# Kernel tuning notes

Hardware: AMD Instinct MI355X
Metric: run time of the kernel (lower is better)

## Reference

```python
import jax, jax.numpy as jnp
import numpy as np

HIDDEN = 896
NUM_Q_HEADS = 14
NUM_KV_HEADS = 2
HEAD_DIM = 64
ROPE_BASE = 10000.0
B, S = 4, 2048


def rotate_half(x):
    x1, x2 = jnp.split(x, 2, axis=-1)
    return jnp.concatenate((-x2, x1), axis=-1)


def rope_cos_sin(position_ids):
    # position_ids: [B, S] int -> cos/sin [B, 1, S, HEAD_DIM]
    inv_freq = 1.0 / (ROPE_BASE ** (jnp.arange(0, HEAD_DIM, 2, dtype=jnp.float32) / HEAD_DIM))
    freqs = position_ids.astype(jnp.float32)[..., None] * inv_freq  # [B,S,D/2]
    emb = jnp.concatenate((freqs, freqs), axis=-1)  # [B,S,D]
    return jnp.cos(emb)[:, None, :, :], jnp.sin(emb)[:, None, :, :]


def setup_inputs() -> dict:
    key = jax.random.key(0)
    k1, k2, k3, k4, k5 = jax.random.split(key, 5)
    s = 1.0 / np.sqrt(HIDDEN)
    return {
        "hidden_states": jax.random.normal(k1, (B, S, HIDDEN), dtype=jnp.float32),
        "position_ids": jnp.broadcast_to(jnp.arange(S, dtype=jnp.int64), (B, S)),
        "Wq": jax.random.normal(k2, (HIDDEN, NUM_Q_HEADS * HEAD_DIM), dtype=jnp.float32) * s,
        "Wk": jax.random.normal(k3, (HIDDEN, NUM_KV_HEADS * HEAD_DIM), dtype=jnp.float32) * s,
        "Wv": jax.random.normal(k4, (HIDDEN, NUM_KV_HEADS * HEAD_DIM), dtype=jnp.float32) * s,
        "Wo": jax.random.normal(k5, (NUM_Q_HEADS * HEAD_DIM, HIDDEN), dtype=jnp.float32) * s,
    }


def reference(hidden_states, position_ids, Wq, Wk, Wv, Wo):
    b, s, _ = hidden_states.shape
    n_rep = NUM_Q_HEADS // NUM_KV_HEADS

    q = (hidden_states @ Wq).reshape(b, s, NUM_Q_HEADS, HEAD_DIM).transpose(0, 2, 1, 3)   # [B,Hq,S,D]
    k = (hidden_states @ Wk).reshape(b, s, NUM_KV_HEADS, HEAD_DIM).transpose(0, 2, 1, 3)  # [B,Hkv,S,D]
    v = (hidden_states @ Wv).reshape(b, s, NUM_KV_HEADS, HEAD_DIM).transpose(0, 2, 1, 3)

    cos, sin = rope_cos_sin(position_ids)  # [B,1,S,D]
    q = q * cos + rotate_half(q) * sin
    k = k * cos + rotate_half(k) * sin

    # repeat_interleave KV heads to match query heads
    k = jnp.repeat(k, n_rep, axis=1)  # [B,Hq,S,D]
    v = jnp.repeat(v, n_rep, axis=1)

    scale = 1.0 / jnp.sqrt(jnp.float32(HEAD_DIM))
    attn = jnp.einsum('bhqd,bhkd->bhqk', q, k) * scale  # [B,Hq,S,S]
    attn = jax.nn.softmax(attn, axis=-1)
    out = jnp.einsum('bhqk,bhkd->bhqd', attn, v)  # [B,Hq,S,D]
    out = out.transpose(0, 2, 1, 3).reshape(b, s, NUM_Q_HEADS * HEAD_DIM)
    return out @ Wo
```

## Files before the change

kernel.cpp:

```cpp
#include <hip/hip_runtime.h>
#include <hip/hip_bf16.h>
#include <math.h>

typedef unsigned short ushort_t;
typedef __bf16 bf16x8 __attribute__((ext_vector_type(8)));
typedef float f32x4 __attribute__((ext_vector_type(4)));

#define HIDDEN 896
#define NQH 14
#define NKVH 2
#define HD 64
#define SEQ 2048
#define NBATCH 4

__device__ inline ushort_t f2bf(float x) {
  union { float f; unsigned u; } c; c.f = x;
  unsigned r = c.u + 0x7FFFu + ((c.u >> 16) & 1u);
  return (ushort_t)(r >> 16);
}

__device__ inline unsigned pack2bf(float a, float b) {
  union { float f; unsigned u; } ca, cb; ca.f = a; cb.f = b;
  unsigned ua = ca.u + 0x8000u, ub = cb.u + 0x8000u;
  return __builtin_amdgcn_perm(ub, ua, 0x07060302);
}

__device__ inline bf16x8 ldfrag(const ushort_t* p) {
  return *reinterpret_cast<const bf16x8*>(p);
}

__device__ inline void async16(const ushort_t* g, ushort_t* l) {
  __builtin_amdgcn_global_load_lds(
      (const __attribute__((address_space(1))) void*)g,
      (__attribute__((address_space(3))) void*)l, 16, 0, 0);
}


__global__ void k_convert(const float* __restrict__ in, ushort_t* __restrict__ out, int n4) {
  int i = blockIdx.x * blockDim.x + threadIdx.x;
  if (i >= n4) return;
  float4 v = reinterpret_cast<const float4*>(in)[i];
  ushort4 o;
  o.x = f2bf(v.x); o.y = f2bf(v.y); o.z = f2bf(v.z); o.w = f2bf(v.w);
  reinterpret_cast<ushort4*>(out)[i] = o;
}

__global__ void k_transpose(const float* __restrict__ in, ushort_t* __restrict__ out, int K, int N) {
  __shared__ float tile[32][33];
  int k0 = blockIdx.y * 32, n0 = blockIdx.x * 32;
  for (int r = threadIdx.y; r < 32; r += 8) {
    int k = k0 + r, n = n0 + threadIdx.x;
    tile[r][threadIdx.x] = (k < K && n < N) ? in[(size_t)k * N + n] : 0.f;
  }
  __syncthreads();
  for (int r = threadIdx.y; r < 32; r += 8) {
    int n = n0 + r, k = k0 + threadIdx.x;
    if (n < N && k < K) out[(size_t)n * K + k] = f2bf(tile[threadIdx.x][r]);
  }
}

__global__ __launch_bounds__(256) void k_qkv(
    const ushort_t* __restrict__ hb,
    const ushort_t* __restrict__ wqT,
    const ushort_t* __restrict__ wkT,
    const ushort_t* __restrict__ wvT,
    const int* __restrict__ pos_ids,
    ushort_t* __restrict__ Qg,
    ushort_t* __restrict__ Kg,
    ushort_t* __restrict__ Vtg) {
  __shared__ ushort_t sa[128 * 32];
  __shared__ ushort_t sb[64 * 32];
  __shared__ float cbuf[128 * 64];

  const int nt = blockIdx.x;
  const int m0 = blockIdx.y * 128;
  const int tid = threadIdx.x;
  const int wave = tid >> 6, lane = tid & 63;
  const int l15 = lane & 15, quad = lane >> 4;
  const int wm = wave >> 1, wn = wave & 1;

  const ushort_t* wsrc; int nsrc0;
  if (nt < 14)      { wsrc = wqT; nsrc0 = nt * 64; }
  else if (nt < 16) { wsrc = wkT; nsrc0 = (nt - 14) * 64; }
  else              { wsrc = wvT; nsrc0 = (nt - 16) * 64; }

  f32x4 acc[4][2];
  const f32x4 z4 = {0.f, 0.f, 0.f, 0.f};
#pragma unroll
  for (int a = 0; a < 4; ++a)
#pragma unroll
    for (int b = 0; b < 2; ++b) acc[a][b] = z4;

  for (int kt = 0; kt < 28; ++kt) {
    const int k0 = kt * 32;
    __syncthreads();
#pragma unroll
    for (int i = 0; i < 2; ++i) {
      int c = wave * 128 + i * 64 + lane;
      async16(hb + (size_t)(m0 + (c >> 2)) * HIDDEN + k0 + (c & 3) * 8,
              sa + (size_t)(wave * 128 + i * 64) * 8);
    }
    {
      int c = wave * 64 + lane;
      async16(wsrc + (size_t)(nsrc0 + (c >> 2)) * HIDDEN + k0 + (c & 3) * 8,
              sb + (size_t)(wave * 64) * 8);
    }
    __syncthreads();
    bf16x8 bf0 = ldfrag(sb + ((wn * 32 + l15) * 32 + quad * 8));
    bf16x8 bf1 = ldfrag(sb + ((wn * 32 + 16 + l15) * 32 + quad * 8));
#pragma unroll
    for (int mb = 0; mb < 4; ++mb) {
      bf16x8 af = ldfrag(sa + ((wm * 64 + mb * 16 + l15) * 32 + quad * 8));
      acc[mb][0] = __builtin_amdgcn_mfma_f32_16x16x32_bf16(af, bf0, acc[mb][0], 0, 0, 0);
      acc[mb][1] = __builtin_amdgcn_mfma_f32_16x16x32_bf16(af, bf1, acc[mb][1], 0, 0, 0);
    }
  }

  __syncthreads();
#pragma unroll
  for (int mb = 0; mb < 4; ++mb)
#pragma unroll
    for (int nb = 0; nb < 2; ++nb)
#pragma unroll
      for (int r = 0; r < 4; ++r)
        cbuf[(wm * 64 + mb * 16 + quad * 4 + r) * 64 + wn * 32 + nb * 16 + l15] = acc[mb][nb][r];
  __syncthreads();

  if (nt < 16) {
    const float cs = 0.125f * 1.44269504088896f;
    for (int p = tid; p < 128 * 32; p += 256) {
      int row = p >> 5, d = p & 31;
      int token = m0 + row;
      int b = token >> 11, s = token & 2047;
      int pos = pos_ids[token];
      float x0 = cbuf[row * 64 + d];
      float x1 = cbuf[row * 64 + d + 32];
      float inv = exp2f(-(float)d * 0.41524101186092596f);
      float ang = (float)pos * inv;
      float sn, cn;
      sincosf(ang, &sn, &cn);
      float y0 = x0 * cn - x1 * sn;
      float y1 = x1 * cn + x0 * sn;
      if (nt < 14) {
        size_t base = ((size_t)(b * NQH + nt) * SEQ + s) * HD;
        Qg[base + d]      = f2bf(y0 * cs);
        Qg[base + d + 32] = f2bf(y1 * cs);
      } else {
        size_t base = ((size_t)(b * NKVH + (nt - 14)) * SEQ + s) * HD;
        Kg[base + d]      = f2bf(y0);
        Kg[base + d + 32] = f2bf(y1);
      }
    }
  } else {
    int kvh = nt - 16;
    for (int p = tid; p < 128 * 64; p += 256) {
      int srow = p & 127, d = p >> 7;
      int token = m0 + srow;
      int b = token >> 11, s = token & 2047;
      Vtg[((size_t)(b * NKVH + kvh) * HD + d) * SEQ + s] = f2bf(cbuf[srow * 64 + d]);
    }
  }
}

__global__ __launch_bounds__(256) void k_attn(
    const ushort_t* __restrict__ Qg,
    const ushort_t* __restrict__ Kg,
    const ushort_t* __restrict__ Vtg,
    ushort_t* __restrict__ attn) {
  __shared__ ushort_t kbuf[64 * 64];
  __shared__ ushort_t vbuf[64 * 64];
  __shared__ ushort_t pbuf[4][32 * 72];

  const int qt = blockIdx.x;
  const int bh = blockIdx.y;
  const int b = bh / NQH, h = bh % NQH;
  const int kvh = h / (NQH / NKVH);
  const int tid = threadIdx.x;
  const int wave = tid >> 6, lane = tid & 63;
  const int l15 = lane & 15, quad = lane >> 4;
  const int q0 = qt * 128;

  bf16x8 qf[2][2];
#pragma unroll
  for (int qs = 0; qs < 2; ++qs) {
    const size_t qb = ((size_t)bh * SEQ + q0 + wave * 32 + qs * 16 + l15) * HD + quad * 8;
    qf[qs][0] = ldfrag(Qg + qb);
    qf[qs][1] = ldfrag(Qg + qb + 32);
  }

  const size_t kbase = (size_t)(b * NKVH + kvh) * SEQ * HD;
  const size_t vbase = (size_t)(b * NKVH + kvh) * HD * SEQ;

  float l_acc[2] = {0.f, 0.f};
  f32x4 o[2][4];
  const f32x4 z4 = {0.f, 0.f, 0.f, 0.f};
#pragma unroll
  for (int qs = 0; qs < 2; ++qs)
#pragma unroll
    for (int nb = 0; nb < 4; ++nb) o[qs][nb] = z4;

  ushort_t* pw = pbuf[wave];

  for (int jt = 0; jt < 32; ++jt) {
    const int s0 = jt * 64;
    __syncthreads();
#pragma unroll
    for (int i = 0; i < 2; ++i) {
      int s = i * 256 + tid;
      int row = s >> 3;
      int c = (s & 7) ^ (row & 7);
      int sbase = i * 256 + wave * 64;
      async16(Kg + kbase + (size_t)(s0 + row) * HD + c * 8, kbuf + sbase * 8);
      async16(Vtg + vbase + (size_t)row * SEQ + s0 + c * 8, vbuf + sbase * 8);
    }
    __syncthreads();

    float lsum[2] = {0.f, 0.f};
#pragma unroll
    for (int nb = 0; nb < 4; ++nb) {
      int row = nb * 16 + l15;
      int sw = row & 7;
      bf16x8 kf0 = ldfrag(kbuf + (row * 8 + (quad ^ sw)) * 8);
      bf16x8 kf1 = ldfrag(kbuf + (row * 8 + ((4 + quad) ^ sw)) * 8);
#pragma unroll
      for (int qs = 0; qs < 2; ++qs) {
        f32x4 t = z4;
        t = __builtin_amdgcn_mfma_f32_16x16x32_bf16(kf0, qf[qs][0], t, 0, 0, 0);
        t = __builtin_amdgcn_mfma_f32_16x16x32_bf16(kf1, qf[qs][1], t, 0, 0, 0);
        float p0 = __builtin_amdgcn_exp2f(t[0]);
        float p1 = __builtin_amdgcn_exp2f(t[1]);
        float p2 = __builtin_amdgcn_exp2f(t[2]);
        float p3 = __builtin_amdgcn_exp2f(t[3]);
        lsum[qs] += (p0 + p1) + (p2 + p3);
        uint2 d;
        d.x = pack2bf(p0, p1);
        d.y = pack2bf(p2, p3);
        *reinterpret_cast<uint2*>(pw + (qs * 16 + l15) * 72 + nb * 16 + quad * 4) = d;
      }
    }
#pragma unroll
    for (int qs = 0; qs < 2; ++qs) {
      float s = lsum[qs];
      s += __shfl_xor(s, 16);
      s += __shfl_xor(s, 32);
      l_acc[qs] += s;
    }

    bf16x8 pf[2][2];
#pragma unroll
    for (int qs = 0; qs < 2; ++qs) {
      pf[qs][0] = ldfrag(pw + (qs * 16 + l15) * 72 + quad * 8);
      pf[qs][1] = ldfrag(pw + (qs * 16 + l15) * 72 + 32 + quad * 8);
    }
#pragma unroll
    for (int nb = 0; nb < 4; ++nb) {
      int row = nb * 16 + l15;
      int sw = row & 7;
      bf16x8 vf0 = ldfrag(vbuf + (row * 8 + (quad ^ sw)) * 8);
      bf16x8 vf1 = ldfrag(vbuf + (row * 8 + ((4 + quad) ^ sw)) * 8);
#pragma unroll
      for (int qs = 0; qs < 2; ++qs) {
        o[qs][nb] = __builtin_amdgcn_mfma_f32_16x16x32_bf16(pf[qs][0], vf0, o[qs][nb], 0, 0, 0);
        o[qs][nb] = __builtin_amdgcn_mfma_f32_16x16x32_bf16(pf[qs][1], vf1, o[qs][nb], 0, 0, 0);
      }
    }
  }

#pragma unroll
  for (int qs = 0; qs < 2; ++qs) {
    float il = 1.0f / l_acc[qs];
#pragma unroll
    for (int r = 0; r < 4; ++r) {
      float inv = __shfl(il, quad * 4 + r);
      int qg = q0 + wave * 32 + qs * 16 + quad * 4 + r;
#pragma unroll
      for (int nb = 0; nb < 4; ++nb) {
        float val = o[qs][nb][r] * inv;
        attn[(size_t)(b * SEQ + qg) * (NQH * HD) + h * HD + nb * 16 + l15] = f2bf(val);
      }
    }
  }
}

__global__ __launch_bounds__(256) void k_oproj(
    const ushort_t* __restrict__ attn,
    const ushort_t* __restrict__ woT,
    float* __restrict__ out) {
  __shared__ ushort_t sa[128 * 32];
  __shared__ ushort_t sb[64 * 32];

  const int n0 = blockIdx.x * 64;
  const int m0 = blockIdx.y * 128;
  const int tid = threadIdx.x;
  const int wave = tid >> 6, lane = tid & 63;
  const int l15 = lane & 15, quad = lane >> 4;
  const int wm = wave >> 1, wn = wave & 1;

  f32x4 acc[4][2];
  const f32x4 z4 = {0.f, 0.f, 0.f, 0.f};
#pragma unroll
  for (int a = 0; a < 4; ++a)
#pragma unroll
    for (int b = 0; b < 2; ++b) acc[a][b] = z4;

  for (int kt = 0; kt < 28; ++kt) {
    const int k0 = kt * 32;
    __syncthreads();
#pragma unroll
    for (int i = 0; i < 2; ++i) {
      int c = wave * 128 + i * 64 + lane;
      async16(attn + (size_t)(m0 + (c >> 2)) * HIDDEN + k0 + (c & 3) * 8,
              sa + (size_t)(wave * 128 + i * 64) * 8);
    }
    {
      int c = wave * 64 + lane;
      async16(woT + (size_t)(n0 + (c >> 2)) * HIDDEN + k0 + (c & 3) * 8,
              sb + (size_t)(wave * 64) * 8);
    }
    __syncthreads();
    bf16x8 bf0 = ldfrag(sb + ((wn * 32 + l15) * 32 + quad * 8));
    bf16x8 bf1 = ldfrag(sb + ((wn * 32 + 16 + l15) * 32 + quad * 8));
#pragma unroll
    for (int mb = 0; mb < 4; ++mb) {
      bf16x8 af = ldfrag(sa + ((wm * 64 + mb * 16 + l15) * 32 + quad * 8));
      acc[mb][0] = __builtin_amdgcn_mfma_f32_16x16x32_bf16(af, bf0, acc[mb][0], 0, 0, 0);
      acc[mb][1] = __builtin_amdgcn_mfma_f32_16x16x32_bf16(af, bf1, acc[mb][1], 0, 0, 0);
    }
  }

#pragma unroll
  for (int mb = 0; mb < 4; ++mb)
#pragma unroll
    for (int nb = 0; nb < 2; ++nb)
#pragma unroll
      for (int r = 0; r < 4; ++r)
        out[(size_t)(m0 + wm * 64 + mb * 16 + quad * 4 + r) * HIDDEN +
            n0 + wn * 32 + nb * 16 + l15] = acc[mb][nb][r];
}


extern "C" void kernel_launch(void* const* d_in, const int* in_sizes, int n_in,
                              void* d_out, int out_size, void* d_ws, size_t ws_size,
                              hipStream_t stream) {
  (void)in_sizes; (void)n_in; (void)out_size; (void)ws_size;
  const float* hidden = (const float*)d_in[0];
  const int* pos      = (const int*)d_in[1];
  const float* Wq     = (const float*)d_in[2];
  const float* Wk     = (const float*)d_in[3];
  const float* Wv     = (const float*)d_in[4];
  const float* Wo     = (const float*)d_in[5];
  float* out = (float*)d_out;

  char* ws = (char*)d_ws;
  ushort_t* hb   = (ushort_t*)(ws);
  ushort_t* wqT  = (ushort_t*)(ws + 14680064);
  ushort_t* wkT  = (ushort_t*)(ws + 16285696);
  ushort_t* wvT  = (ushort_t*)(ws + 16515072);
  ushort_t* woT  = (ushort_t*)(ws + 16744448);
  ushort_t* Qg   = (ushort_t*)(ws + 18350080);
  ushort_t* Kg   = (ushort_t*)(ws + 33030144);
  ushort_t* Vtg  = (ushort_t*)(ws + 35127296);
  ushort_t* attn = (ushort_t*)(ws + 37224448);

  k_convert<<<7168, 256, 0, stream>>>(hidden, hb, 1835008);
  dim3 tb(32, 8);
  k_transpose<<<dim3(28, 28), tb, 0, stream>>>(Wq, wqT, 896, 896);
  k_transpose<<<dim3(4, 28), tb, 0, stream>>>(Wk, wkT, 896, 128);
  k_transpose<<<dim3(4, 28), tb, 0, stream>>>(Wv, wvT, 896, 128);
  k_transpose<<<dim3(28, 28), tb, 0, stream>>>(Wo, woT, 896, 896);

  k_qkv<<<dim3(18, 64), 256, 0, stream>>>(hb, wqT, wkT, wvT, pos, Qg, Kg, Vtg);
  k_attn<<<dim3(16, 56), 256, 0, stream>>>(Qg, Kg, Vtg, attn);
  k_oproj<<<dim3(14, 64), 256, 0, stream>>>(attn, woT, out);
}
```

Baseline: 269.8 us.

## Merge prep kernels, widen GEMM tiles, use RoPE table, double-buffer attention KV

Folds the conversion and all weight transposes into one launch that also precomputes a cos/sin table. The QKV and output-projection GEMMs move to 128x128 tiles, and the QKV epilogue applies RoPE straight from registers, dropping the LDS staging buffer and the per-element sincos. Attention now double-buffers its K/V tiles so the next tile loads while the current one is computed, and defers the row-sum reduction to the end. The aim is fewer launches, more reuse per tile and less load latency, in exchange for higher register and LDS pressure that could lower occupancy. The cos/sin table is indexed by the pos value and holds only 2048 entries, so position ids outside that range would read past it.

```diff
diff --git a/kernel.cpp b/kernel.cpp
--- a/kernel.cpp
+++ b/kernel.cpp
@@ -36,18 +36,10 @@
 }
 
 
-__global__ void k_convert(const float* __restrict__ in, ushort_t* __restrict__ out, int n4) {
-  int i = blockIdx.x * blockDim.x + threadIdx.x;
-  if (i >= n4) return;
-  float4 v = reinterpret_cast<const float4*>(in)[i];
-  ushort4 o;
-  o.x = f2bf(v.x); o.y = f2bf(v.y); o.z = f2bf(v.z); o.w = f2bf(v.w);
-  reinterpret_cast<ushort4*>(out)[i] = o;
-}
-
-__global__ void k_transpose(const float* __restrict__ in, ushort_t* __restrict__ out, int K, int N) {
+__device__ inline void transpose_sec(const float* __restrict__ in, ushort_t* __restrict__ out,
+                                     int K, int N, int bx, int by) {
   __shared__ float tile[32][33];
-  int k0 = blockIdx.y * 32, n0 = blockIdx.x * 32;
+  int k0 = by * 32, n0 = bx * 32;
   for (int r = threadIdx.y; r < 32; r += 8) {
     int k = k0 + r, n = n0 + threadIdx.x;
     tile[r][threadIdx.x] = (k < K && n < N) ? in[(size_t)k * N + n] : 0.f;
@@ -59,37 +51,67 @@
   }
 }
 
+__global__ void k_prep(const float* __restrict__ hidden, ushort_t* __restrict__ hb,
+                       const float* __restrict__ Wq, const float* __restrict__ Wk,
+                       const float* __restrict__ Wv, const float* __restrict__ Wo,
+                       ushort_t* __restrict__ wT, ushort_t* __restrict__ woT,
+                       float2* __restrict__ ctab) {
+  const int blk = blockIdx.x;
+  const int tid = threadIdx.y * 32 + threadIdx.x;
+  if (blk < 7168) {
+    int i = blk * 256 + tid;
+    float4 v = reinterpret_cast<const float4*>(hidden)[i];
+    ushort4 o;
+    o.x = f2bf(v.x); o.y = f2bf(v.y); o.z = f2bf(v.z); o.w = f2bf(v.w);
+    reinterpret_cast<ushort4*>(hb)[i] = o;
+  } else if (blk < 7424) {
+    int idx = (blk - 7168) * 256 + tid;
+    int s = idx >> 5, dp = idx & 31;
+    float inv = exp2f(-(float)dp * 0.41524101186092596f);
+    float ang = (float)s * inv;
+    float sn, cn;
+    sincosf(ang, &sn, &cn);
+    ctab[idx] = make_float2(cn, sn);
+  } else if (blk < 8208) {
+    int t = blk - 7424;
+    transpose_sec(Wq, wT, 896, 896, t % 28, t / 28);
+  } else if (blk < 8320) {
+    int t = blk - 8208;
+    transpose_sec(Wk, wT + (size_t)896 * 896, 896, 128, t % 4, t / 4);
+  } else if (blk < 8432) {
+    int t = blk - 8320;
+    transpose_sec(Wv, wT + (size_t)1024 * 896, 896, 128, t % 4, t / 4);
+  } else {
+    int t = blk - 8432;
+    transpose_sec(Wo, woT, 896, 896, t % 28, t / 28);
+  }
+}
+
 __global__ __launch_bounds__(256) void k_qkv(
     const ushort_t* __restrict__ hb,
-    const ushort_t* __restrict__ wqT,
-    const ushort_t* __restrict__ wkT,
-    const ushort_t* __restrict__ wvT,
+    const ushort_t* __restrict__ wT,
     const int* __restrict__ pos_ids,
+    const float2* __restrict__ ctab,
     ushort_t* __restrict__ Qg,
     ushort_t* __restrict__ Kg,
     ushort_t* __restrict__ Vtg) {
   __shared__ ushort_t sa[128 * 32];
-  __shared__ ushort_t sb[64 * 32];
-  __shared__ float cbuf[128 * 64];
-
-  const int nt = blockIdx.x;
+  __shared__ ushort_t sbb[128 * 32];
+
+  const int sect = blockIdx.x;
+  const int nt0 = sect * 128;
   const int m0 = blockIdx.y * 128;
   const int tid = threadIdx.x;
   const int wave = tid >> 6, lane = tid & 63;
   const int l15 = lane & 15, quad = lane >> 4;
   const int wm = wave >> 1, wn = wave & 1;
 
-  const ushort_t* wsrc; int nsrc0;
-  if (nt < 14)      { wsrc = wqT; nsrc0 = nt * 64; }
-  else if (nt < 16) { wsrc = wkT; nsrc0 = (nt - 14) * 64; }
-  else              { wsrc = wvT; nsrc0 = (nt - 16) * 64; }
-
-  f32x4 acc[4][2];
+  f32x4 acc[4][4];
   const f32x4 z4 = {0.f, 0.f, 0.f, 0.f};
 #pragma unroll
   for (int a = 0; a < 4; ++a)
 #pragma unroll
-    for (int b = 0; b < 2; ++b) acc[a][b] = z4;
+    for (int b = 0; b < 4; ++b) acc[a][b] = z4;
 
   for (int kt = 0; kt < 28; ++kt) {
     const int k0 = kt * 32;
@@ -99,65 +121,62 @@
       int c = wave * 128 + i * 64 + lane;
       async16(hb + (size_t)(m0 + (c >> 2)) * HIDDEN + k0 + (c & 3) * 8,
               sa + (size_t)(wave * 128 + i * 64) * 8);
-    }
-    {
-      int c = wave * 64 + lane;
-      async16(wsrc + (size_t)(nsrc0 + (c >> 2)) * HIDDEN + k0 + (c & 3) * 8,
-              sb + (size_t)(wave * 64) * 8);
+      async16(wT + (size_t)(nt0 + (c >> 2)) * HIDDEN + k0 + (c & 3) * 8,
+              sbb + (size_t)(wave * 128 + i * 64) * 8);
     }
     __syncthreads();
-    bf16x8 bf0 = ldfrag(sb + ((wn * 32 + l15) * 32 + quad * 8));
-    bf16x8 bf1 = ldfrag(sb + ((wn * 32 + 16 + l15) * 32 + quad * 8));
+    bf16x8 bf[4], af[4];
+#pragma unroll
+    for (int nb = 0; nb < 4; ++nb)
+      bf[nb] = ldfrag(sbb + ((wn * 64 + nb * 16 + l15) * 32 + quad * 8));
+#pragma unroll
+    for (int mb = 0; mb < 4; ++mb)
+      af[mb] = ldfrag(sa + ((wm * 64 + mb * 16 + l15) * 32 + quad * 8));
+#pragma unroll
+    for (int mb = 0; mb < 4; ++mb)
+#pragma unroll
+      for (int nb = 0; nb < 4; ++nb)
+        acc[mb][nb] = __builtin_amdgcn_mfma_f32_16x16x32_bf16(af[mb], bf[nb], acc[mb][nb], 0, 0, 0);
+  }
+
+  if (sect < 8) {
+    const bool isQ = sect < 7;
+    const float csc = isQ ? 0.125f * 1.4426950408889634f : 1.0f;
+    ushort_t* dst = isQ ? Qg : Kg;
+    const int nheads = isQ ? NQH : NKVH;
+    const int hh = isQ ? sect * 2 + wn : wn;
+#pragma unroll
+    for (int mb = 0; mb < 4; ++mb)
+#pragma unroll
+      for (int r = 0; r < 4; ++r) {
+        int token = m0 + wm * 64 + mb * 16 + quad * 4 + r;
+        int b = token >> 11, s = token & 2047;
+        int pos = pos_ids[token];
+        size_t base = ((size_t)(b * nheads + hh) * SEQ + s) * HD;
+#pragma unroll
+        for (int nb = 0; nb < 2; ++nb) {
+          float2 cs = ctab[pos * 32 + nb * 16 + l15];
+          float x0 = acc[mb][nb][r];
+          float x1 = acc[mb][nb + 2][r];
+          float y0 = (x0 * cs.x - x1 * cs.y) * csc;
+          float y1 = (x1 * cs.x + x0 * cs.y) * csc;
+          dst[base + nb * 16 + l15]      = f2bf(y0);
+          dst[base + nb * 16 + l15 + 32] = f2bf(y1);
+        }
+      }
+  } else {
 #pragma unroll
     for (int mb = 0; mb < 4; ++mb) {
-      bf16x8 af = ldfrag(sa + ((wm * 64 + mb * 16 + l15) * 32 + quad * 8));
-      acc[mb][0] = __builtin_amdgcn_mfma_f32_16x16x32_bf16(af, bf0, acc[mb][0], 0, 0, 0);
-      acc[mb][1] = __builtin_amdgcn_mfma_f32_16x16x32_bf16(af, bf1, acc[mb][1], 0, 0, 0);
-    }
-  }
-
-  __syncthreads();
-#pragma unroll
-  for (int mb = 0; mb < 4; ++mb)
-#pragma unroll
-    for (int nb = 0; nb < 2; ++nb)
-#pragma unroll
-      for (int r = 0; r < 4; ++r)
-        cbuf[(wm * 64 + mb * 16 + quad * 4 + r) * 64 + wn * 32 + nb * 16 + l15] = acc[mb][nb][r];
-  __syncthreads();
-
-  if (nt < 16) {
-    const float cs = 0.125f * 1.44269504088896f;
-    for (int p = tid; p < 128 * 32; p += 256) {
-      int row = p >> 5, d = p & 31;
-      int token = m0 + row;
-      int b = token >> 11, s = token & 2047;
-      int pos = pos_ids[token];
-      float x0 = cbuf[row * 64 + d];
-      float x1 = cbuf[row * 64 + d + 32];
-      float inv = exp2f(-(float)d * 0.41524101186092596f);
-      float ang = (float)pos * inv;
-      float sn, cn;
-      sincosf(ang, &sn, &cn);
-      float y0 = x0 * cn - x1 * sn;
-      float y1 = x1 * cn + x0 * sn;
-      if (nt < 14) {
-        size_t base = ((size_t)(b * NQH + nt) * SEQ + s) * HD;
-        Qg[base + d]      = f2bf(y0 * cs);
-        Qg[base + d + 32] = f2bf(y1 * cs);
-      } else {
-        size_t base = ((size_t)(b * NKVH + (nt - 14)) * SEQ + s) * HD;
-        Kg[base + d]      = f2bf(y0);
-        Kg[base + d + 32] = f2bf(y1);
+      int token0 = m0 + wm * 64 + mb * 16 + quad * 4;
+      int b = token0 >> 11, s = token0 & 2047;
+#pragma unroll
+      for (int nb = 0; nb < 4; ++nb) {
+        int d = nb * 16 + l15;
+        uint2 pk;
+        pk.x = pack2bf(acc[mb][nb][0], acc[mb][nb][1]);
+        pk.y = pack2bf(acc[mb][nb][2], acc[mb][nb][3]);
+        *reinterpret_cast<uint2*>(Vtg + ((size_t)(b * NKVH + wn) * HD + d) * SEQ + s) = pk;
       }
-    }
-  } else {
-    int kvh = nt - 16;
-    for (int p = tid; p < 128 * 64; p += 256) {
-      int srow = p & 127, d = p >> 7;
-      int token = m0 + srow;
-      int b = token >> 11, s = token & 2047;
-      Vtg[((size_t)(b * NKVH + kvh) * HD + d) * SEQ + s] = f2bf(cbuf[srow * 64 + d]);
     }
   }
 }
@@ -167,8 +186,8 @@
     const ushort_t* __restrict__ Kg,
     const ushort_t* __restrict__ Vtg,
     ushort_t* __restrict__ attn) {
-  __shared__ ushort_t kbuf[64 * 64];
-  __shared__ ushort_t vbuf[64 * 64];
+  __shared__ ushort_t kbuf[2][64 * 64];
+  __shared__ ushort_t vbuf[2][64 * 64];
   __shared__ ushort_t pbuf[4][32 * 72];
 
   const int qt = blockIdx.x;
@@ -191,7 +210,14 @@
   const size_t kbase = (size_t)(b * NKVH + kvh) * SEQ * HD;
   const size_t vbase = (size_t)(b * NKVH + kvh) * HD * SEQ;
 
-  float l_acc[2] = {0.f, 0.f};
+  const int srow = tid >> 3;
+  const int sc0 = (tid & 7) ^ (srow & 7);
+  const int srow2 = (256 + tid) >> 3;
+  const int sc2 = (tid & 7) ^ (srow2 & 7);
+  const int sbase1 = wave * 64 * 8;
+  const int sbase2 = (256 + wave * 64) * 8;
+
+  float l_part[2] = {0.f, 0.f};
   f32x4 o[2][4];
   const f32x4 z4 = {0.f, 0.f, 0.f, 0.f};
 #pragma unroll
@@ -201,27 +227,32 @@
 
   ushort_t* pw = pbuf[wave];
 
+  async16(Kg + kbase + (size_t)srow * HD + sc0 * 8, kbuf[0] + sbase1);
+  async16(Vtg + vbase + (size_t)srow * SEQ + sc0 * 8, vbuf[0] + sbase1);
+  async16(Kg + kbase + (size_t)srow2 * HD + sc2 * 8, kbuf[0] + sbase2);
+  async16(Vtg + vbase + (size_t)srow2 * SEQ + sc2 * 8, vbuf[0] + sbase2);
+
   for (int jt = 0; jt < 32; ++jt) {
-    const int s0 = jt * 64;
+    const int cur = jt & 1;
     __syncthreads();
-#pragma unroll
-    for (int i = 0; i < 2; ++i) {
-      int s = i * 256 + tid;
-      int row = s >> 3;
-      int c = (s & 7) ^ (row & 7);
-      int sbase = i * 256 + wave * 64;
-      async16(Kg + kbase + (size_t)(s0 + row) * HD + c * 8, kbuf + sbase * 8);
-      async16(Vtg + vbase + (size_t)row * SEQ + s0 + c * 8, vbuf + sbase * 8);
-    }
-    __syncthreads();
-
-    float lsum[2] = {0.f, 0.f};
+    if (jt + 1 < 32) {
+      const int nxt = cur ^ 1;
+      const int s1 = (jt + 1) * 64;
+      async16(Kg + kbase + (size_t)(s1 + srow) * HD + sc0 * 8, kbuf[nxt] + sbase1);
+      async16(Vtg + vbase + (size_t)srow * SEQ + s1 + sc0 * 8, vbuf[nxt] + sbase1);
+      async16(Kg + kbase + (size_t)(s1 + srow2) * HD + sc2 * 8, kbuf[nxt] + sbase2);
+      async16(Vtg + vbase + (size_t)srow2 * SEQ + s1 + sc2 * 8, vbuf[nxt] + sbase2);
+    }
+
+    const ushort_t* kb = kbuf[cur];
+    const ushort_t* vb = vbuf[cur];
+
 #pragma unroll
     for (int nb = 0; nb < 4; ++nb) {
       int row = nb * 16 + l15;
       int sw = row & 7;
-      bf16x8 kf0 = ldfrag(kbuf + (row * 8 + (quad ^ sw)) * 8);
-      bf16x8 kf1 = ldfrag(kbuf + (row * 8 + ((4 + quad) ^ sw)) * 8);
+      bf16x8 kf0 = ldfrag(kb + (row * 8 + (quad ^ sw)) * 8);
+      bf16x8 kf1 = ldfrag(kb + (row * 8 + ((4 + quad) ^ sw)) * 8);
 #pragma unroll
       for (int qs = 0; qs < 2; ++qs) {
         f32x4 t = z4;
@@ -231,20 +262,13 @@
         float p1 = __builtin_amdgcn_exp2f(t[1]);
         float p2 = __builtin_amdgcn_exp2f(t[2]);
         float p3 = __builtin_amdgcn_exp2f(t[3]);
-        lsum[qs] += (p0 + p1) + (p2 + p3);
+        l_part[qs] += (p0 + p1) + (p2 + p3);
         uint2 d;
         d.x = pack2bf(p0, p1);
         d.y = pack2bf(p2, p3);
         *reinterpret_cast<uint2*>(pw + (qs * 16 + l15) * 72 + nb * 16 + quad * 4) = d;
       }
     }
-#pragma unroll
-    for (int qs = 0; qs < 2; ++qs) {
-      float s = lsum[qs];
-      s += __shfl_xor(s, 16);
-      s += __shfl_xor(s, 32);
-      l_acc[qs] += s;
-    }
 
     bf16x8 pf[2][2];
 #pragma unroll
@@ -256,8 +280,8 @@
     for (int nb = 0; nb < 4; ++nb) {
       int row = nb * 16 + l15;
       int sw = row & 7;
-      bf16x8 vf0 = ldfrag(vbuf + (row * 8 + (quad ^ sw)) * 8);
-      bf16x8 vf1 = ldfrag(vbuf + (row * 8 + ((4 + quad) ^ sw)) * 8);
+      bf16x8 vf0 = ldfrag(vb + (row * 8 + (quad ^ sw)) * 8);
+      bf16x8 vf1 = ldfrag(vb + (row * 8 + ((4 + quad) ^ sw)) * 8);
 #pragma unroll
       for (int qs = 0; qs < 2; ++qs) {
         o[qs][nb] = __builtin_amdgcn_mfma_f32_16x16x32_bf16(pf[qs][0], vf0, o[qs][nb], 0, 0, 0);
@@ -268,7 +292,15 @@
 
 #pragma unroll
   for (int qs = 0; qs < 2; ++qs) {
-    float il = 1.0f / l_acc[qs];
+    float s = l_part[qs];
+    s += __shfl_xor(s, 16);
+    s += __shfl_xor(s, 32);
+    l_part[qs] = s;
+  }
+
+#pragma unroll
+  for (int qs = 0; qs < 2; ++qs) {
+    float il = 1.0f / l_part[qs];
 #pragma unroll
     for (int r = 0; r < 4; ++r) {
       float inv = __shfl(il, quad * 4 + r);
@@ -287,21 +319,21 @@
     const ushort_t* __restrict__ woT,
     float* __restrict__ out) {
   __shared__ ushort_t sa[128 * 32];
-  __shared__ ushort_t sb[64 * 32];
-
-  const int n0 = blockIdx.x * 64;
+  __shared__ ushort_t sbb[128 * 32];
+
+  const int n0 = blockIdx.x * 128;
   const int m0 = blockIdx.y * 128;
   const int tid = threadIdx.x;
   const int wave = tid >> 6, lane = tid & 63;
   const int l15 = lane & 15, quad = lane >> 4;
   const int wm = wave >> 1, wn = wave & 1;
 
-  f32x4 acc[4][2];
+  f32x4 acc[4][4];
   const f32x4 z4 = {0.f, 0.f, 0.f, 0.f};
 #pragma unroll
   for (int a = 0; a < 4; ++a)
 #pragma unroll
-    for (int b = 0; b < 2; ++b) acc[a][b] = z4;
+    for (int b = 0; b < 4; ++b) acc[a][b] = z4;
 
   for (int kt = 0; kt < 28; ++kt) {
     const int k0 = kt * 32;
@@ -311,31 +343,32 @@
       int c = wave * 128 + i * 64 + lane;
       async16(attn + (size_t)(m0 + (c >> 2)) * HIDDEN + k0 + (c & 3) * 8,
               sa + (size_t)(wave * 128 + i * 64) * 8);
-    }
-    {
-      int c = wave * 64 + lane;
       async16(woT + (size_t)(n0 + (c >> 2)) * HIDDEN + k0 + (c & 3) * 8,
-              sb + (size_t)(wave * 64) * 8);
+              sbb + (size_t)(wave * 128 + i * 64) * 8);
     }
     __syncthreads();
-    bf16x8 bf0 = ldfrag(sb + ((wn * 32 + l15) * 32 + quad * 8));
-    bf16x8 bf1 = ldfrag(sb + ((wn * 32 + 16 + l15) * 32 + quad * 8));
-#pragma unroll
-    for (int mb = 0; mb < 4; ++mb) {
-      bf16x8 af = ldfrag(sa + ((wm * 64 + mb * 16 + l15) * 32 + quad * 8));
-      acc[mb][0] = __builtin_amdgcn_mfma_f32_16x16x32_bf16(af, bf0, acc[mb][0], 0, 0, 0);
-      acc[mb][1] = __builtin_amdgcn_mfma_f32_16x16x32_bf16(af, bf1, acc[mb][1], 0, 0, 0);
-    }
+    bf16x8 bf[4], af[4];
+#pragma unroll
+    for (int nb = 0; nb < 4; ++nb)
+      bf[nb] = ldfrag(sbb + ((wn * 64 + nb * 16 + l15) * 32 + quad * 8));
+#pragma unroll
+    for (int mb = 0; mb < 4; ++mb)
+      af[mb] = ldfrag(sa + ((wm * 64 + mb * 16 + l15) * 32 + quad * 8));
+#pragma unroll
+    for (int mb = 0; mb < 4; ++mb)
+#pragma unroll
+      for (int nb = 0; nb < 4; ++nb)
+        acc[mb][nb] = __builtin_amdgcn_mfma_f32_16x16x32_bf16(af[mb], bf[nb], acc[mb][nb], 0, 0, 0);
   }
 
 #pragma unroll
   for (int mb = 0; mb < 4; ++mb)
 #pragma unroll
-    for (int nb = 0; nb < 2; ++nb)
+    for (int nb = 0; nb < 4; ++nb)
 #pragma unroll
       for (int r = 0; r < 4; ++r)
         out[(size_t)(m0 + wm * 64 + mb * 16 + quad * 4 + r) * HIDDEN +
-            n0 + wn * 32 + nb * 16 + l15] = acc[mb][nb][r];
+            n0 + wn * 64 + nb * 16 + l15] = acc[mb][nb][r];
 }
 
 
@@ -353,23 +386,16 @@
 
   char* ws = (char*)d_ws;
   ushort_t* hb   = (ushort_t*)(ws);
-  ushort_t* wqT  = (ushort_t*)(ws + 14680064);
-  ushort_t* wkT  = (ushort_t*)(ws + 16285696);
-  ushort_t* wvT  = (ushort_t*)(ws + 16515072);
-  ushort_t* woT  = (ushort_t*)(ws + 16744448);
-  ushort_t* Qg   = (ushort_t*)(ws + 18350080);
-  ushort_t* Kg   = (ushort_t*)(ws + 33030144);
-  ushort_t* Vtg  = (ushort_t*)(ws + 35127296);
-  ushort_t* attn = (ushort_t*)(ws + 37224448);
-
-  k_convert<<<7168, 256, 0, stream>>>(hidden, hb, 1835008);
-  dim3 tb(32, 8);
-  k_transpose<<<dim3(28, 28), tb, 0, stream>>>(Wq, wqT, 896, 896);
-  k_transpose<<<dim3(4, 28), tb, 0, stream>>>(Wk, wkT, 896, 128);
-  k_transpose<<<dim3(4, 28), tb, 0, stream>>>(Wv, wvT, 896, 128);
-  k_transpose<<<dim3(28, 28), tb, 0, stream>>>(Wo, woT, 896, 896);
-
-  k_qkv<<<dim3(18, 64), 256, 0, stream>>>(hb, wqT, wkT, wvT, pos, Qg, Kg, Vtg);
+  ushort_t* wT   = (ushort_t*)(ws + 14680064);
+  float2*   ctab = (float2*)  (ws + 16744448);
+  ushort_t* Qg   = (ushort_t*)(ws + 17268736);
+  ushort_t* Kg   = (ushort_t*)(ws + 31948800);
+  ushort_t* Vtg  = (ushort_t*)(ws + 34045952);
+  ushort_t* attn = (ushort_t*)(ws + 36143104);
+  ushort_t* woT  = (ushort_t*)(ws + 50823168);
+
+  k_prep<<<9216, dim3(32, 8), 0, stream>>>(hidden, hb, Wq, Wk, Wv, Wo, wT, woT, ctab);
+  k_qkv<<<dim3(9, 64), 256, 0, stream>>>(hb, wT, pos, ctab, Qg, Kg, Vtg);
   k_attn<<<dim3(16, 56), 256, 0, stream>>>(Qg, Kg, Vtg, attn);
-  k_oproj<<<dim3(14, 64), 256, 0, stream>>>(attn, woT, out);
-}
+  k_oproj<<<dim3(7, 64), 256, 0, stream>>>(attn, woT, out);
+}
```

Measured after the change: 270.3 us. Within noise of the previous version (+0.2%).
